# Kernel tuning notes

Measured on AMD Instinct MI355X. Metric: run time of the kernel, lower is better.

Reference implementation:

```python
import jax, jax.numpy as jnp
import numpy as np

N_HEAD = 8
N_FEAT = 512
D_HEAD = N_FEAT // N_HEAD


def setup_inputs() -> dict:
    key = jax.random.key(0)
    ks = jax.random.split(key, 11)
    B, T, L = 4, 2048, 16
    s = 1.0 / np.sqrt(D_HEAD)
    so = 1.0 / np.sqrt(N_FEAT)
    return {
        "q": jax.random.normal(ks[0], (B, T, 1, N_FEAT), jnp.float32),
        "k": jax.random.normal(ks[1], (B, T, L, N_FEAT), jnp.float32),
        "v": jax.random.normal(ks[2], (B, T, L, N_FEAT), jnp.float32),
        "Wq": jax.random.uniform(ks[3], (D_HEAD, D_HEAD), jnp.float32, -s, s),
        "bq": jax.random.uniform(ks[4], (D_HEAD,), jnp.float32, -s, s),
        "Wk": jax.random.uniform(ks[5], (D_HEAD, D_HEAD), jnp.float32, -s, s),
        "bk": jax.random.uniform(ks[6], (D_HEAD,), jnp.float32, -s, s),
        "Wv": jax.random.uniform(ks[7], (D_HEAD, D_HEAD), jnp.float32, -s, s),
        "bv": jax.random.uniform(ks[8], (D_HEAD,), jnp.float32, -s, s),
        "Wo": jax.random.uniform(ks[9], (N_FEAT, N_FEAT), jnp.float32, -so, so),
        "bo": jax.random.uniform(ks[10], (N_FEAT,), jnp.float32, -so, so),
    }


def reference(q, k, v, Wq, bq, Wk, bk, Wv, bv, Wo, bo):
    B, T, L, F = k.shape
    H, D = N_HEAD, D_HEAD
    # split heads: q [B,T,H,D] (query axis of length 1 squeezed), k/v [B,T,L,H,D]
    qh = q.reshape(B, T, H, D)
    kh = k.reshape(B, T, L, H, D)
    vh = v.reshape(B, T, L, H, D)
    # per-head linear projections (shared across heads), Linear: x @ W^T + b
    qh = jnp.einsum("bthd,ed->bthe", qh, Wq) + bq
    kh = jnp.einsum("btlhd,ed->btlhe", kh, Wk) + bk
    vh = jnp.einsum("btlhd,ed->btlhe", vh, Wv) + bv
    # attention scores over the local window L (query length 1 per timestep)
    attw = jnp.einsum("bthd,btlhd->bthl", qh, kh) / jnp.sqrt(jnp.asarray(D, qh.dtype))
    attn = jax.nn.softmax(attw, axis=-1)  # dropout is identity in eval mode
    ct = jnp.einsum("bthl,btlhd->bthd", attn, vh)
    ct = ct.reshape(B, T, F)
    return ct @ Wo.T + bo
```

## Files before the change

kernel.cpp:

```cpp
#include <hip/hip_runtime.h>


#define NFEAT 512
#define NHEAD 8
#define DHEAD 64
#define LWIN  16
#define WPOS  8
#define FBT   8
#define VPITCH 520

typedef __attribute__((ext_vector_type(8))) short bf16x8;
typedef __attribute__((ext_vector_type(4))) float f32x4;

__device__ __forceinline__ unsigned short f2bf(float f) {
    unsigned int u = __float_as_uint(f);
    unsigned int r = (u + 0x7fffu + ((u >> 16) & 1u)) >> 16;
    return (unsigned short)r;
}

__global__ void precompute_small(const float* __restrict__ Wq, const float* __restrict__ bq,
                                 const float* __restrict__ Wk,
                                 const float* __restrict__ Wo, const float* __restrict__ bo,
                                 const float* __restrict__ bv,
                                 float* __restrict__ A, float* __restrict__ g,
                                 float* __restrict__ b2) {
    int idx = blockIdx.x * 256 + threadIdx.x;
    if (idx < 4096) {
        int d = idx >> 6, dp = idx & 63;
        float s = 0.f;
        #pragma unroll 8
        for (int e = 0; e < 64; ++e) s = fmaf(Wq[e * 64 + d], Wk[e * 64 + dp], s);
        A[idx] = s;
    } else if (idx < 4160) {
        int dp = idx - 4096;
        float s = 0.f;
        #pragma unroll 8
        for (int e = 0; e < 64; ++e) s = fmaf(Wk[e * 64 + dp], bq[e], s);
        g[dp] = s;
    } else if (idx < 4672) {
        int j = idx - 4160;
        float s = bo[j];
        #pragma unroll 8
        for (int i = 0; i < 512; ++i) s = fmaf(Wo[j * 512 + i], bv[i & 63], s);
        b2[j] = s;
    }
}

__global__ void precompute_wo2(const float* __restrict__ Wo, const float* __restrict__ Wv,
                               unsigned short* __restrict__ Wo2B) {
    int idx = blockIdx.x * 256 + threadIdx.x;
    int i = idx & 511, j = idx >> 9;
    int h = i >> 6, e = i & 63;
    float s = 0.f;
    #pragma unroll 8
    for (int d = 0; d < 64; ++d)
        s = fmaf(Wo[j * 512 + h * 64 + d], Wv[d * 64 + e], s);
    Wo2B[(size_t)j * 512 + i] = f2bf(s);
}

__global__ __launch_bounds__(512, 4)
void w_prepass(const float* __restrict__ q, const float* __restrict__ A,
               const float* __restrict__ g, float* __restrict__ Wm) {
    __shared__ float As[4096];
    __shared__ float qs[WPOS][NFEAT];
    const int tid = threadIdx.x;
    const int bt0 = blockIdx.x * WPOS;

    #pragma unroll
    for (int i = 0; i < 8; ++i) As[i * 512 + tid] = A[i * 512 + tid];
    #pragma unroll
    for (int r = 0; r < WPOS; ++r) qs[r][tid] = q[(size_t)(bt0 + r) * NFEAT + tid];
    __syncthreads();

    const int e  = tid & 63;
    const int hb = (tid >> 6) << 6;
    float acc[WPOS];
    const float ge = g[e];
    #pragma unroll
    for (int r = 0; r < WPOS; ++r) acc[r] = ge;

    #pragma unroll 4
    for (int dq = 0; dq < 16; ++dq) {
        const float a0 = As[(4 * dq + 0) * 64 + e];
        const float a1 = As[(4 * dq + 1) * 64 + e];
        const float a2 = As[(4 * dq + 2) * 64 + e];
        const float a3 = As[(4 * dq + 3) * 64 + e];
        #pragma unroll
        for (int r = 0; r < WPOS; ++r) {
            const float4 qv = *reinterpret_cast<const float4*>(&qs[r][hb + 4 * dq]);
            acc[r] = fmaf(qv.x, a0, acc[r]);
            acc[r] = fmaf(qv.y, a1, acc[r]);
            acc[r] = fmaf(qv.z, a2, acc[r]);
            acc[r] = fmaf(qv.w, a3, acc[r]);
        }
    }
    #pragma unroll
    for (int r = 0; r < WPOS; ++r)
        Wm[(size_t)(bt0 + r) * NFEAT + tid] = acc[r] * 0.125f;
}

__global__ __launch_bounds__(512, 8)
void attn_fused(const float* __restrict__ Wm, const float* __restrict__ k,
                const float* __restrict__ v, const unsigned short* __restrict__ Wo2B,
                const float* __restrict__ b2, float* __restrict__ out) {
    __shared__ float ps[NHEAD][FBT][17];
    __shared__ __align__(16) unsigned short vbarS[FBT * VPITCH];

    const int tid = threadIdx.x;
    const int bt0 = blockIdx.x * FBT;

    {
        const int h    = tid >> 6;
        const int lane = tid & 63;
        const int l    = lane >> 2;
        const int d4   = lane & 3;
        const int off  = h * 64 + d4 * 16;

        for (int p = 0; p < FBT; ++p) {
            const float4* w4 = reinterpret_cast<const float4*>(
                Wm + (size_t)(bt0 + p) * NFEAT + off);
            const float4* k4 = reinterpret_cast<const float4*>(
                k + (size_t)(bt0 + p) * (LWIN * NFEAT) + (size_t)l * NFEAT + off);
            float a0 = 0.f, a1 = 0.f, a2 = 0.f, a3 = 0.f;
            #pragma unroll
            for (int i = 0; i < 4; ++i) {
                const float4 wq = w4[i];
                const float4 kq = k4[i];
                a0 = fmaf(wq.x, kq.x, a0);
                a1 = fmaf(wq.y, kq.y, a1);
                a2 = fmaf(wq.z, kq.z, a2);
                a3 = fmaf(wq.w, kq.w, a3);
            }
            float sc = (a0 + a1) + (a2 + a3);
            sc += __shfl_xor(sc, 1, 64);
            sc += __shfl_xor(sc, 2, 64);
            const float e = __expf(sc);
            if (d4 == 0) ps[h][p][l] = e;
        }
    }
    __syncthreads();

    {
        const int pq = tid >> 7;
        const int f4 = tid & 127;
        const int hh = f4 >> 4;
        #pragma unroll
        for (int ii = 0; ii < FBT / 4; ++ii) {
            const int bt = ii * 4 + pq;
            float pv[LWIN];
            #pragma unroll
            for (int i = 0; i < LWIN; ++i) pv[i] = ps[hh][bt][i];
            float s0 = (pv[0] + pv[1]) + (pv[2] + pv[3]);
            float s1 = (pv[4] + pv[5]) + (pv[6] + pv[7]);
            float s2 = (pv[8] + pv[9]) + (pv[10] + pv[11]);
            float s3 = (pv[12] + pv[13]) + (pv[14] + pv[15]);
            const float inv = 1.0f / ((s0 + s1) + (s2 + s3));

            const float4* vp = reinterpret_cast<const float4*>(
                v + (size_t)(bt0 + bt) * (LWIN * NFEAT)) + f4;
            float ax = 0.f, ay = 0.f, az = 0.f, aw = 0.f;
            #pragma unroll
            for (int l = 0; l < LWIN; ++l) {
                const float4 vv = vp[(size_t)l * 128];
                ax = fmaf(pv[l], vv.x, ax);
                ay = fmaf(pv[l], vv.y, ay);
                az = fmaf(pv[l], vv.z, az);
                aw = fmaf(pv[l], vv.w, aw);
            }
            ax *= inv; ay *= inv; az *= inv; aw *= inv;
            unsigned short o[4] = { f2bf(ax), f2bf(ay), f2bf(az), f2bf(aw) };
            *reinterpret_cast<uint2*>(vbarS + bt * VPITCH + f4 * 4) =
                *reinterpret_cast<uint2*>(o);
        }
    }
    __syncthreads();

    {
        const int w    = tid >> 6;
        const int lane = tid & 63;
        const int n0   = w * 64;
        const int r    = lane & 15;
        const int kg   = lane >> 4;

        const unsigned short* As0 = vbarS + (r & 7) * VPITCH + kg * 8;
        const short* Bb0 = (const short*)Wo2B + ((size_t)(n0 +  0 + r)) * 512 + kg * 8;
        const short* Bb1 = (const short*)Wo2B + ((size_t)(n0 + 16 + r)) * 512 + kg * 8;
        const short* Bb2 = (const short*)Wo2B + ((size_t)(n0 + 32 + r)) * 512 + kg * 8;
        const short* Bb3 = (const short*)Wo2B + ((size_t)(n0 + 48 + r)) * 512 + kg * 8;

        f32x4 acc0 = {0.f, 0.f, 0.f, 0.f}, acc1 = acc0, acc2 = acc0, acc3 = acc0;

        #pragma unroll 4
        for (int kk = 0; kk < 16; ++kk) {
            const bf16x8 a   = *reinterpret_cast<const bf16x8*>(As0 + kk * 32);
            const bf16x8 b0  = *reinterpret_cast<const bf16x8*>(Bb0 + kk * 32);
            const bf16x8 b1  = *reinterpret_cast<const bf16x8*>(Bb1 + kk * 32);
            const bf16x8 b2v = *reinterpret_cast<const bf16x8*>(Bb2 + kk * 32);
            const bf16x8 b3  = *reinterpret_cast<const bf16x8*>(Bb3 + kk * 32);
            acc0 = __builtin_amdgcn_mfma_f32_16x16x32_bf16(a, b0,  acc0, 0, 0, 0);
            acc1 = __builtin_amdgcn_mfma_f32_16x16x32_bf16(a, b1,  acc1, 0, 0, 0);
            acc2 = __builtin_amdgcn_mfma_f32_16x16x32_bf16(a, b2v, acc2, 0, 0, 0);
            acc3 = __builtin_amdgcn_mfma_f32_16x16x32_bf16(a, b3,  acc3, 0, 0, 0);
        }

        if (kg < 2) {
            const float bb0 = b2[n0 + 0 + r],  bb1 = b2[n0 + 16 + r];
            const float bb2 = b2[n0 + 32 + r], bb3 = b2[n0 + 48 + r];
            #pragma unroll
            for (int j = 0; j < 4; ++j) {
                const size_t row = (size_t)(bt0 + kg * 4 + j) * 512;
                out[row + n0 +  0 + r] = acc0[j] + bb0;
                out[row + n0 + 16 + r] = acc1[j] + bb1;
                out[row + n0 + 32 + r] = acc2[j] + bb2;
                out[row + n0 + 48 + r] = acc3[j] + bb3;
            }
        }
    }
}

extern "C" void kernel_launch(void* const* d_in, const int* in_sizes, int n_in,
                              void* d_out, int out_size, void* d_ws, size_t ws_size,
                              hipStream_t stream) {
    const float* q  = (const float*)d_in[0];
    const float* k  = (const float*)d_in[1];
    const float* v  = (const float*)d_in[2];
    const float* Wq = (const float*)d_in[3];
    const float* bq = (const float*)d_in[4];
    const float* Wk = (const float*)d_in[5];
    const float* Wv = (const float*)d_in[7];
    const float* bv = (const float*)d_in[8];
    const float* Wo = (const float*)d_in[9];
    const float* bo = (const float*)d_in[10];
    float* out = (float*)d_out;

    float* ws = (float*)d_ws;
    float*          A    = ws;
    float*          g    = ws + 4096;
    float*          b2   = ws + 4160;
    unsigned short* Wo2B = (unsigned short*)(ws + 4672);
    float*          Wm   = ws + 4672 + 131072;

    const int BT = in_sizes[0] / NFEAT;

    hipLaunchKernelGGL(precompute_small, dim3(19), dim3(256), 0, stream,
                       Wq, bq, Wk, Wo, bo, bv, A, g, b2);
    hipLaunchKernelGGL(precompute_wo2, dim3(1024), dim3(256), 0, stream,
                       Wo, Wv, Wo2B);
    hipLaunchKernelGGL(w_prepass, dim3(BT / WPOS), dim3(512), 0, stream,
                       q, A, g, Wm);
    hipLaunchKernelGGL(attn_fused, dim3(BT / FBT), dim3(512), 0, stream,
                       Wm, k, v, Wo2B, b2, out);
}
```

Measured before the change: 209.7 us.

## Assign one wave per timestep and fuse scores, softmax and V-weighting in registers

The score, softmax and weighted-V stages are restructured so that each wavefront owns one timestep. Each lane covers 8 features (two float4 halves), reduces scores with 16-lane shuffles and keeps the exp weights in registers. This removes the shared-memory score buffer and one block barrier, and lets every lane issue all K and V loads for its timestep up front. The launch-bounds occupancy hint drops from 8 to 4 to leave room for the larger register footprint.

```diff
diff --git a/kernel.cpp b/kernel.cpp
--- a/kernel.cpp
+++ b/kernel.cpp
@@ -99,79 +99,60 @@
         Wm[(size_t)(bt0 + r) * NFEAT + tid] = acc[r] * 0.125f;
 }
 
-__global__ __launch_bounds__(512, 8)
+__global__ __launch_bounds__(512, 4)
 void attn_fused(const float* __restrict__ Wm, const float* __restrict__ k,
                 const float* __restrict__ v, const unsigned short* __restrict__ Wo2B,
                 const float* __restrict__ b2, float* __restrict__ out) {
-    __shared__ float ps[NHEAD][FBT][17];
     __shared__ __align__(16) unsigned short vbarS[FBT * VPITCH];
 
     const int tid = threadIdx.x;
-    const int bt0 = blockIdx.x * FBT;
-
+    const int wv  = tid >> 6;
+    const int j   = tid & 63;
+    const int bt  = blockIdx.x * FBT + wv;
+
+    const float4 wa = *reinterpret_cast<const float4*>(Wm + (size_t)bt * NFEAT + j * 4);
+    const float4 wb = *reinterpret_cast<const float4*>(Wm + (size_t)bt * NFEAT + 256 + j * 4);
+
+    const float* kbase = k + (size_t)bt * (LWIN * NFEAT);
+    float e0[LWIN], e1[LWIN];
+    float den0 = 0.f, den1 = 0.f;
+    #pragma unroll
+    for (int l = 0; l < LWIN; ++l) {
+        const float4 ka = *reinterpret_cast<const float4*>(kbase + l * NFEAT + j * 4);
+        const float4 kb = *reinterpret_cast<const float4*>(kbase + l * NFEAT + 256 + j * 4);
+        float pa = wa.x * ka.x, pb = wb.x * kb.x;
+        pa = fmaf(wa.y, ka.y, pa);  pb = fmaf(wb.y, kb.y, pb);
+        pa = fmaf(wa.z, ka.z, pa);  pb = fmaf(wb.z, kb.z, pb);
+        pa = fmaf(wa.w, ka.w, pa);  pb = fmaf(wb.w, kb.w, pb);
+        pa += __shfl_xor(pa, 1, 64);  pb += __shfl_xor(pb, 1, 64);
+        pa += __shfl_xor(pa, 2, 64);  pb += __shfl_xor(pb, 2, 64);
+        pa += __shfl_xor(pa, 4, 64);  pb += __shfl_xor(pb, 4, 64);
+        pa += __shfl_xor(pa, 8, 64);  pb += __shfl_xor(pb, 8, 64);
+        const float ea = __expf(pa);  const float eb = __expf(pb);
+        e0[l] = ea;  den0 += ea;
+        e1[l] = eb;  den1 += eb;
+    }
+    const float inv0 = 1.0f / den0, inv1 = 1.0f / den1;
+
+    const float* vbase = v + (size_t)bt * (LWIN * NFEAT);
+    float a0x = 0.f, a0y = 0.f, a0z = 0.f, a0w = 0.f;
+    float a1x = 0.f, a1y = 0.f, a1z = 0.f, a1w = 0.f;
+    #pragma unroll
+    for (int l = 0; l < LWIN; ++l) {
+        const float4 va = *reinterpret_cast<const float4*>(vbase + l * NFEAT + j * 4);
+        const float4 vb = *reinterpret_cast<const float4*>(vbase + l * NFEAT + 256 + j * 4);
+        a0x = fmaf(e0[l], va.x, a0x);  a1x = fmaf(e1[l], vb.x, a1x);
+        a0y = fmaf(e0[l], va.y, a0y);  a1y = fmaf(e1[l], vb.y, a1y);
+        a0z = fmaf(e0[l], va.z, a0z);  a1z = fmaf(e1[l], vb.z, a1z);
+        a0w = fmaf(e0[l], va.w, a0w);  a1w = fmaf(e1[l], vb.w, a1w);
+    }
     {
-        const int h    = tid >> 6;
-        const int lane = tid & 63;
-        const int l    = lane >> 2;
-        const int d4   = lane & 3;
-        const int off  = h * 64 + d4 * 16;
-
-        for (int p = 0; p < FBT; ++p) {
-            const float4* w4 = reinterpret_cast<const float4*>(
-                Wm + (size_t)(bt0 + p) * NFEAT + off);
-            const float4* k4 = reinterpret_cast<const float4*>(
-                k + (size_t)(bt0 + p) * (LWIN * NFEAT) + (size_t)l * NFEAT + off);
-            float a0 = 0.f, a1 = 0.f, a2 = 0.f, a3 = 0.f;
-            #pragma unroll
-            for (int i = 0; i < 4; ++i) {
-                const float4 wq = w4[i];
-                const float4 kq = k4[i];
-                a0 = fmaf(wq.x, kq.x, a0);
-                a1 = fmaf(wq.y, kq.y, a1);
-                a2 = fmaf(wq.z, kq.z, a2);
-                a3 = fmaf(wq.w, kq.w, a3);
-            }
-            float sc = (a0 + a1) + (a2 + a3);
-            sc += __shfl_xor(sc, 1, 64);
-            sc += __shfl_xor(sc, 2, 64);
-            const float e = __expf(sc);
-            if (d4 == 0) ps[h][p][l] = e;
-        }
-    }
-    __syncthreads();
-
-    {
-        const int pq = tid >> 7;
-        const int f4 = tid & 127;
-        const int hh = f4 >> 4;
-        #pragma unroll
-        for (int ii = 0; ii < FBT / 4; ++ii) {
-            const int bt = ii * 4 + pq;
-            float pv[LWIN];
-            #pragma unroll
-            for (int i = 0; i < LWIN; ++i) pv[i] = ps[hh][bt][i];
-            float s0 = (pv[0] + pv[1]) + (pv[2] + pv[3]);
-            float s1 = (pv[4] + pv[5]) + (pv[6] + pv[7]);
-            float s2 = (pv[8] + pv[9]) + (pv[10] + pv[11]);
-            float s3 = (pv[12] + pv[13]) + (pv[14] + pv[15]);
-            const float inv = 1.0f / ((s0 + s1) + (s2 + s3));
-
-            const float4* vp = reinterpret_cast<const float4*>(
-                v + (size_t)(bt0 + bt) * (LWIN * NFEAT)) + f4;
-            float ax = 0.f, ay = 0.f, az = 0.f, aw = 0.f;
-            #pragma unroll
-            for (int l = 0; l < LWIN; ++l) {
-                const float4 vv = vp[(size_t)l * 128];
-                ax = fmaf(pv[l], vv.x, ax);
-                ay = fmaf(pv[l], vv.y, ay);
-                az = fmaf(pv[l], vv.z, az);
-                aw = fmaf(pv[l], vv.w, aw);
-            }
-            ax *= inv; ay *= inv; az *= inv; aw *= inv;
-            unsigned short o[4] = { f2bf(ax), f2bf(ay), f2bf(az), f2bf(aw) };
-            *reinterpret_cast<uint2*>(vbarS + bt * VPITCH + f4 * 4) =
-                *reinterpret_cast<uint2*>(o);
-        }
+        unsigned short oa[4] = { f2bf(a0x * inv0), f2bf(a0y * inv0),
+                                 f2bf(a0z * inv0), f2bf(a0w * inv0) };
+        unsigned short ob[4] = { f2bf(a1x * inv1), f2bf(a1y * inv1),
+                                 f2bf(a1z * inv1), f2bf(a1w * inv1) };
+        *reinterpret_cast<uint2*>(vbarS + wv * VPITCH + j * 4)       = *reinterpret_cast<uint2*>(oa);
+        *reinterpret_cast<uint2*>(vbarS + wv * VPITCH + 256 + j * 4) = *reinterpret_cast<uint2*>(ob);
     }
     __syncthreads();
 
@@ -204,15 +185,16 @@
         }
 
         if (kg < 2) {
+            const int bt0 = blockIdx.x * FBT;
             const float bb0 = b2[n0 + 0 + r],  bb1 = b2[n0 + 16 + r];
             const float bb2 = b2[n0 + 32 + r], bb3 = b2[n0 + 48 + r];
             #pragma unroll
-            for (int j = 0; j < 4; ++j) {
-                const size_t row = (size_t)(bt0 + kg * 4 + j) * 512;
-                out[row + n0 +  0 + r] = acc0[j] + bb0;
-                out[row + n0 + 16 + r] = acc1[j] + bb1;
-                out[row + n0 + 32 + r] = acc2[j] + bb2;
-                out[row + n0 + 48 + r] = acc3[j] + bb3;
+            for (int jj = 0; jj < 4; ++jj) {
+                const size_t row = (size_t)(bt0 + kg * 4 + jj) * 512;
+                out[row + n0 +  0 + r] = acc0[jj] + bb0;
+                out[row + n0 + 16 + r] = acc1[jj] + bb1;
+                out[row + n0 + 32 + r] = acc2[jj] + bb2;
+                out[row + n0 + 48 + r] = acc3[jj] + bb3;
             }
         }
     }
```

Result: faster. 199.8 us (-4.7%).
